# Performance work log

Measured on AMD Instinct MI355X. Metric: run time of the kernel, lower is better.

The kernel has to match this reference:

```python
import jax, jax.numpy as jnp
import numpy as np

# dims
B, H, W = 2, 128, 256
MD = 34            # model_dim (last 2 channels = sin/cos lat)
LD = MD - 2        # learnable_dim = 32
NH, HD = 4, 8      # n_heads, head_dim
SH = 64            # shared_hidden (DISCO out channels)
K = 25             # number of DISCO basis functions (5x5 kernel_shape)
P = 7              # local stencil width (lat x lon support of geodesic basis)
R = P // 2
FF1, FF2 = 512, 256


def setup_inputs() -> dict:
    key = jax.random.key(0)
    ks = jax.random.split(key, 16)
    x = jax.random.normal(ks[0], (B, H, W, MD), dtype=jnp.float32)
    # latitude-dependent sparse geodesic basis values over a 7x7 stencil
    psi_val = jax.random.uniform(ks[1], (K, H, P * P), dtype=jnp.float32) * 0.1
    disco_w = jax.random.normal(ks[2], (SH, K), dtype=jnp.float32) * 0.1
    disco_b = jax.random.normal(ks[3], (SH,), dtype=jnp.float32) * 0.01
    # per-head MLP: shared_hidden -> 32 -> 1
    hw1 = jax.random.normal(ks[4], (NH, SH, 32), dtype=jnp.float32) * (1.0 / np.sqrt(SH))
    hb1 = jax.random.normal(ks[5], (NH, 32), dtype=jnp.float32) * 0.01
    hw2 = jax.random.normal(ks[6], (NH, 32, 1), dtype=jnp.float32) * (1.0 / np.sqrt(32))
    hb2 = jax.random.normal(ks[7], (NH, 1), dtype=jnp.float32) * 0.01
    # FFN: model_dim -> 512 -> 256 -> learnable_dim
    fw1 = jax.random.normal(ks[8], (MD, FF1), dtype=jnp.float32) * (1.0 / np.sqrt(MD))
    fw1 = fw1.at[-2:, :].set(0.0)  # matches ffn[0].weight[:, -2:] = 0 init
    fb1 = jax.random.normal(ks[9], (FF1,), dtype=jnp.float32) * 0.01
    fw2 = jax.random.normal(ks[10], (FF1, FF2), dtype=jnp.float32) * (1.0 / np.sqrt(FF1))
    fb2 = jax.random.normal(ks[11], (FF2,), dtype=jnp.float32) * 0.01
    fw3 = jax.random.normal(ks[12], (FF2, LD), dtype=jnp.float32) * (1.0 / np.sqrt(FF2))
    fb3 = jax.random.normal(ks[13], (LD,), dtype=jnp.float32) * 0.01
    return {"x": x, "psi_val": psi_val, "disco_w": disco_w, "disco_b": disco_b,
            "hw1": hw1, "hb1": hb1, "hw2": hw2, "hb2": hb2,
            "fw1": fw1, "fb1": fb1, "fw2": fw2, "fb2": fb2, "fw3": fw3, "fb3": fb3}


def _gelu(t):
    return jax.nn.gelu(t, approximate=False)  # torch nn.GELU default (erf)


def _disco_s2(xn, psi_val, disco_w, disco_b):
    """DISCO sparse-basis conv on single-channel maps.
    xn: (N, H, W). Basis values vary with output latitude, longitude is
    translation-invariant; support is a lat-clamped / lon-wrapped 7x7 stencil.
    Returns (N, SH, H, W)."""
    xp = jnp.pad(xn, ((0, 0), (R, R), (0, 0)), mode="edge")  # clamp at poles
    shifts = []
    for dlat in range(P):
        row = xp[:, dlat:dlat + H, :]
        for dlon in range(-R, R + 1):
            shifts.append(jnp.roll(row, -dlon, axis=2))  # wrap in longitude
    xs = jnp.stack(shifts, axis=1)  # (N, P*P, H, W)
    basis = jnp.einsum("khp,nphw->nkhw", psi_val, xs)       # basis aggregation
    return jnp.einsum("fk,nkhw->nfhw", disco_w, basis) + disco_b[None, :, None, None]


def reference(x, psi_val, disco_w, disco_b, hw1, hb1, hw2, hb2,
              fw1, fb1, fw2, fb2, fw3, fb3):
    x_learn = x[..., :LD]
    sin_cos = x[..., LD:]
    x_res = x_learn
    # (B,H,W,LD) -> (B*LD, H, W): each learnable channel is a 1-channel map
    xn = x_learn.transpose(0, 3, 1, 2).reshape(B * LD, H, W)
    d = _disco_s2(xn, psi_val, disco_w, disco_b)              # (B*LD, SH, H, W)
    d = d.reshape(B, LD, SH, H, W).transpose(0, 3, 4, 1, 2)    # (B,H,W,LD,SH)
    # per-head MLP over its head_dim slice (head index is outer in LD)
    d = d.reshape(B, H, W, NH, HD, SH)
    h = _gelu(jnp.einsum("bxynds,nso->bxyndo", d, hw1) + hb1[None, None, None, :, None, :])
    h = jnp.einsum("bxyndo,noe->bxynde", h, hw2) + hb2[None, None, None, :, None, :]
    x_learn = h[..., 0].reshape(B, H, W, LD)
    x_learn = x_learn + x_res                                  # use_residual
    x_full = jnp.concatenate([x_learn, sin_cos], axis=-1)
    x_res2 = x_learn
    t = _gelu(x_full @ fw1 + fb1)
    t = _gelu(t @ fw2 + fb2)
    t = t @ fw3 + fb3                                          # dropout p=0 -> id
    x_learn = t + x_res2
    return jnp.concatenate([x_learn, sin_cos], axis=-1)
```

## Files before the change

kernel.cpp:

```cpp
#include <hip/hip_runtime.h>
#include <math.h>


typedef __attribute__((ext_vector_type(8))) short bfrag;
typedef __attribute__((ext_vector_type(4))) float ffrag;
typedef __attribute__((ext_vector_type(4))) short short4v;

union bfi4 { int4 i; bfrag b; };

__device__ __forceinline__ float gelu_f(float v) {
  const float z = v * (2.3022077484f + 0.1029451564f * v * v);
  const float e = __builtin_amdgcn_exp2f(-z);
  return v * __builtin_amdgcn_rcpf(1.0f + e);
}

__device__ __forceinline__ short f2bf(float f) {
  union { float f; unsigned u; } v; v.f = f;
  unsigned r = (v.u + 0x7fffu + ((v.u >> 16) & 1u)) >> 16;
  return (short)r;
}

__device__ __forceinline__ short f2bf_fast(float f) {
  union { float f; unsigned u; } v; v.f = f;
  return (short)((v.u + 0x8000u) >> 16);
}

__device__ __forceinline__ float bf2f(short s) {
  union { float f; unsigned u; } v;
  v.u = ((unsigned)(unsigned short)s) << 16;
  return v.f;
}

__device__ __forceinline__ int pkbf(float a, float b) {
  union { float f; unsigned u; } va, vb; va.f = a; vb.f = b;
  return (int)__builtin_amdgcn_perm(vb.u + 0x8000u, va.u + 0x8000u, 0x07060302u);
}

__device__ __forceinline__ void st4bf(short* p, float4 v) {
  short4v s;
  s[0] = f2bf(v.x); s[1] = f2bf(v.y); s[2] = f2bf(v.z); s[3] = f2bf(v.w);
  *(short4v*)p = s;
}

__device__ __forceinline__ void tile_map(int& w0, int& b, int& h, int& lin) {
  lin  = blockIdx.x + (blockIdx.y << 3) + (blockIdx.z << 10);
  const int xcd  = lin & 7;
  const int slot = lin >> 3;
  w0 = (slot & 7) * 32;
  b  = (slot >> 3) & 1;
  h  = (xcd << 4) | (slot >> 4);
}

__global__ __launch_bounds__(256) void k01_prep(
    const float* __restrict__ psi, const float* __restrict__ dw,
    const float* __restrict__ db,
    const float* __restrict__ fw1, const float* __restrict__ fw2,
    const float* __restrict__ fw3, const float* __restrict__ hw1,
    const float* __restrict__ hb1,
    short* __restrict__ wcb, short* __restrict__ fw1s,
    short* __restrict__ fw2s, short* __restrict__ fw3s) {
  __shared__ __align__(16) char sm[24960];
  const int bid = blockIdx.x;
  const int tid = threadIdx.x;

  if (bid < 512) {
    float* tileL  = (float*)sm;
    float* hw1n   = (float*)(sm + 13312);
    short* tile2  = (short*)(sm + 21504);
    float* bias32 = (float*)(sm + 24832);
    const int h = bid >> 2;
    const int n = bid & 3;
    const int lane = tid & 63;
    const int w = __builtin_amdgcn_readfirstlane(tid >> 6);

    for (int e = tid; e < 512; e += 256)
      ((float4*)hw1n)[e] = ((const float4*)(hw1 + n * 2048))[e];

    float dwreg[25];
#pragma unroll
    for (int kk = 0; kk < 25; ++kk) dwreg[kk] = dw[lane * 25 + kk];
    const int p0 = w * 13;
    const int pend = (p0 + 13 < 49) ? (p0 + 13) : 49;
#pragma unroll 1
    for (int p = p0; p < pend; ++p) {
      float ae = 0.f, ao = 0.f;
#pragma unroll
      for (int kk = 0; kk < 24; kk += 2) {
        ae += dwreg[kk]     * psi[kk * 6272 + h * 49 + p];
        ao += dwreg[kk + 1] * psi[(kk + 1) * 6272 + h * 49 + p];
      }
      ae += dwreg[24] * psi[24 * 6272 + h * 49 + p];
      tileL[lane * 52 + p] = ae + ao;
    }
    __syncthreads();

    if (tid >= 224) {
      const int o = tid - 224;
      float acc = hb1[n * 32 + o];
#pragma unroll 4
      for (int s = 0; s < 64; ++s) acc += hw1n[s * 32 + o] * db[s];
      bias32[o] = acc;
    }

    const int o = tid & 31;
#pragma unroll 1
    for (int pp = tid >> 5; pp < 25; pp += 8) {
      const int p2 = pp * 2;
      float a0 = 0.f, a1 = 0.f, a2 = 0.f, a3 = 0.f;
#pragma unroll 4
      for (int f = 0; f < 64; f += 2) {
        const float wv0 = hw1n[f * 32 + o];
        const float wv1 = hw1n[(f + 1) * 32 + o];
        a0 += wv0 * tileL[f * 52 + p2];
        a1 += wv0 * tileL[f * 52 + p2 + 1];
        a2 += wv1 * tileL[(f + 1) * 52 + p2];
        a3 += wv1 * tileL[(f + 1) * 52 + p2 + 1];
      }
      tile2[o * 52 + p2] = f2bf(a0 + a2);
      if (p2 + 1 < 49) tile2[o * 52 + p2 + 1] = f2bf(a1 + a3);
    }
    __syncthreads();

    short* outp = wcb + h * 16384 + n * 4096;
    for (int idx = tid; idx < 4096; idx += 256) {
      const int jj = idx & 7, ln = (idx >> 3) & 63;
      const int nt = (idx >> 9) & 1, kt = (idx >> 10) & 1;
      const int par = idx >> 11;
      const int k = kt * 32 + ((ln >> 4) << 3) + jj;
      const int oo = nt * 16 + (ln & 15);
      const int r = k >> 3, dlt = k & 7;
      const int j = par ? (dlt - 1) : dlt;
      short v = 0;
      if (r < 7 && j >= 0 && j < 7) v = tile2[oo * 52 + r * 7 + j];
      if (k == 56) v = f2bf(bias32[oo]);
      outp[idx] = v;
    }
    return;
  }

  if (bid < 528) {
    short* S = (short*)sm;
    const int kt = bid - 512;
    const float* src = fw2 + kt * 8192;
    for (int q = tid; q < 2048; q += 256) {
      const int lin = q * 4;
      const int kk = lin >> 8, nn = lin & 255;
      st4bf(S + kk * 260 + nn, *(const float4*)(src + lin));
    }
    __syncthreads();
    short* dst = fw2s + kt * 8192;
    for (int q = tid; q < 8192; q += 256) {
      const int jj = q & 7, lane = (q >> 3) & 63, nt = q >> 9;
      const int kk = (lane >> 4) * 8 + jj, nn = nt * 16 + (lane & 15);
      dst[q] = S[kk * 260 + nn];
    }
    return;
  }

  if (bid < 530) {
    const int X = bid - 528;
    short* S = (short*)sm;
    for (int q = tid; q < 2048; q += 256) {
      const int lin = q * 4;
      const int kk = lin >> 8, nn = lin & 255;
      st4bf(S + kk * 260 + nn, *(const float4*)(fw1 + kk * 512 + X * 256 + nn));
    }
    __syncthreads();
    for (int q = tid; q < 8192; q += 256) {
      const int jj = q & 7, lane = (q >> 3) & 63, ntl = q >> 9;
      const int kk = (lane >> 4) * 8 + jj, nn = ntl * 16 + (lane & 15);
      fw1s[X * 8192 + q] = S[kk * 260 + nn];
    }
    return;
  }

  {
    short* S = (short*)sm;
    for (int q = tid; q < 2048; q += 256) {
      const int lin = q * 4;
      const int kk = lin >> 5, nn = lin & 31;
      st4bf(S + kk * 36 + nn, *(const float4*)(fw3 + lin));
    }
    __syncthreads();
    for (int q = tid; q < 8192; q += 256) {
      const int jj = q & 7, lane = (q >> 3) & 63;
      const int nt = (q >> 9) & 1, kt = q >> 10;
      const int kk = kt * 32 + (lane >> 4) * 8 + jj, nn = nt * 16 + (lane & 15);
      fw3s[q] = S[kk * 36 + nn];
    }
  }
}

__global__ __launch_bounds__(256, 8) void k23_fused(
    const float* __restrict__ x,    const short* __restrict__ wcb,
    const float* __restrict__ hw2,  const float* __restrict__ hb2,
    const short* __restrict__ fw1s, const short* __restrict__ fw2s,
    const short* __restrict__ fw3s,
    const float* __restrict__ fb1,  const float* __restrict__ fb2,
    const float* __restrict__ fb3,  float* __restrict__ outb) {
  __shared__ __align__(16) char smem[20384];
  short* sX = (short*)smem;
  short* sM = (short*)(smem + 18080);

  const int tid = threadIdx.x;
  int w0, b, h, lin;
  tile_map(w0, b, h, lin);

  const int lane = tid & 63, lm = lane & 15, lq = lane >> 4;
  const int n = tid >> 6;
  const int idx16 = (lane ^ 16) << 2;
  const int idx32 = (lane ^ 32) << 2;
  const unsigned injm = (lq == 3) ? 0xFFFFu : 0u;

  const float hb2n = hb2[n];

  {
    int4* p = (int4*)smem;
    int4 z; z.x = z.y = z.z = z.w = 0;
    for (int e = tid; e < 20384 / 16; e += 256) p[e] = z;
  }
  __syncthreads();

#pragma unroll 1
  for (int r = 0; r < 7; ++r) {
    int hr = h - 3 + r; hr = hr < 0 ? 0 : (hr > 127 ? 127 : hr);
    const int slot = (r < 4) ? (2 * r) : (2 * r - 7);
    const float* __restrict__ xrow = x + (size_t)((b * 128 + hr) * 256) * 34;
    short* __restrict__ sxr = sX + slot * 40;
    for (int e = tid; e < 39 * 16; e += 256) {
      const int c2 = e & 15;
      const int wp = e >> 4;
      const int wr = (w0 - 3 + wp) & 255;
      const float2 v = *(const float2*)&xrow[wr * 34 + c2 * 2];
      short* dp = sxr + (c2 * 2) * 280 + wp;
      dp[0]   = f2bf_fast(v.x);
      dp[280] = f2bf_fast(v.y);
    }
  }
  __syncthreads();

  const int* tpB = (const int*)sX;

  const float4 w0v = *(const float4*)(hw2 + n * 32 + lq * 4);
  const float4 w1v = *(const float4*)(hw2 + n * 32 + 16 + lq * 4);

#pragma unroll 1
  for (int par = 0; par < 2; ++par) {
    bfrag cw[2][2];
#pragma unroll
    for (int kt = 0; kt < 2; ++kt)
#pragma unroll
      for (int nt = 0; nt < 2; ++nt)
        cw[kt][nt] = *(const bfrag*)(wcb + h * 16384 + n * 4096 +
                         ((par * 2 + kt) * 2 + nt) * 512 + lane * 8);

#pragma unroll 1
    for (int i = 0; i < 8; ++i) {
      const int c = n * 8 + i;

      const int base0 = c * 140 + lq * 40 + lm;
      bfi4 u0, u1;
      u0.i.x = tpB[base0];      u0.i.y = tpB[base0 + 1];
      u0.i.z = tpB[base0 + 2];  u0.i.w = tpB[base0 + 3];
      u1.i.x = tpB[base0 + 20]; u1.i.y = tpB[base0 + 21];
      u1.i.z = tpB[base0 + 22]; u1.i.w = tpB[base0 + 23];
      u1.i.x = (int)(((unsigned)u1.i.x & ~injm) | (0x3F80u & injm));

      ffrag h0 = {0.f, 0.f, 0.f, 0.f}, h1 = {0.f, 0.f, 0.f, 0.f};
      h0 = __builtin_amdgcn_mfma_f32_16x16x32_bf16(cw[0][0], u0.b, h0, 0, 0, 0);
      h0 = __builtin_amdgcn_mfma_f32_16x16x32_bf16(cw[1][0], u1.b, h0, 0, 0, 0);
      h1 = __builtin_amdgcn_mfma_f32_16x16x32_bf16(cw[0][1], u0.b, h1, 0, 0, 0);
      h1 = __builtin_amdgcn_mfma_f32_16x16x32_bf16(cw[1][1], u1.b, h1, 0, 0, 0);

      float s0 = gelu_f(h0[0]) * w0v.x;
      s0 += gelu_f(h0[1]) * w0v.y;
      s0 += gelu_f(h0[2]) * w0v.z;
      s0 += gelu_f(h0[3]) * w0v.w;
      float s1 = gelu_f(h1[0]) * w1v.x;
      s1 += gelu_f(h1[1]) * w1v.y;
      s1 += gelu_f(h1[2]) * w1v.z;
      s1 += gelu_f(h1[3]) * w1v.w;
      union { float f; int i; } sv, t1, t2;
      sv.f = s0 + s1;
      t1.i = __builtin_amdgcn_ds_bpermute(idx16, sv.i);
      sv.f += t1.f;
      t2.i = __builtin_amdgcn_ds_bpermute(idx32, sv.i);
      const float tot = sv.f + t2.f;

      const int p = 2 * lm + par;
      const float res = bf2f(sX[c * 280 + 243 + p]);
      if (lq == 0) sM[p * 36 + c] = f2bf_fast(tot + hb2n + res);
    }
  }
  __syncthreads();

  short* sT1h = (short*)smem;
  short* sT2  = (short*)smem;
  float* sO   = (float*)smem;
  const int wave = n;
  const int koff = lq * 8;
  const int mt3 = wave & 1;
  const int nt3 = wave >> 1;
  const int col3 = nt3 * 16 + lm;
  const int pixg = (b * 128 + h) * 256 + w0;
  const int n0 = wave * 4;

  ffrag acc[2][4];
#pragma unroll
  for (int mt = 0; mt < 2; ++mt)
#pragma unroll
    for (int ni = 0; ni < 4; ++ni) acc[mt][ni] = ffrag{0.f, 0.f, 0.f, 0.f};
  const short* w2base = fw2s + n0 * 512 + lane * 8;

#pragma unroll 1
  for (int H = 0; H < 2; ++H) {
#pragma unroll
    for (int ni = 0; ni < 4; ++ni) {
      const bfrag b1f = *(const bfrag*)(fw1s +
                          (H * 16 + wave * 4 + ni) * 512 + lane * 8);
      const int ntl = wave * 4 + ni;
      const float4 fb1v = *(const float4*)(fb1 + H * 256 + ntl * 16 + lq * 4);
#pragma unroll
      for (int mt = 0; mt < 2; ++mt) {
        const bfrag aFm = *(const bfrag*)(sM + (mt * 16 + lm) * 36 + koff);
        ffrag cc = {0.f, 0.f, 0.f, 0.f};
        cc = __builtin_amdgcn_mfma_f32_16x16x32_bf16(b1f, aFm, cc, 0, 0, 0);
        int2 wv;
        wv.x = pkbf(gelu_f(cc[0] + fb1v.x), gelu_f(cc[1] + fb1v.y));
        wv.y = pkbf(gelu_f(cc[2] + fb1v.z), gelu_f(cc[3] + fb1v.w));
        *(int2*)(sT1h + (mt * 16 + lm) * 264 + ntl * 16 + lq * 4) = wv;
      }
    }
    __syncthreads();

#pragma unroll 1
    for (int kt = 0; kt < 8; ++kt) {
      const bfrag a0 = *(const bfrag*)(sT1h + lm * 264 + kt * 32 + koff);
      const bfrag a1 = *(const bfrag*)(sT1h + (16 + lm) * 264 + kt * 32 + koff);
#pragma unroll
      for (int np = 0; np < 2; ++np) {
        const bfrag bv0 = *(const bfrag*)(w2base + (H * 8 + kt) * 8192 + (2 * np) * 512);
        const bfrag bv1 = *(const bfrag*)(w2base + (H * 8 + kt) * 8192 + (2 * np + 1) * 512);
        acc[0][2 * np]     = __builtin_amdgcn_mfma_f32_16x16x32_bf16(bv0, a0, acc[0][2 * np], 0, 0, 0);
        acc[1][2 * np]     = __builtin_amdgcn_mfma_f32_16x16x32_bf16(bv0, a1, acc[1][2 * np], 0, 0, 0);
        acc[0][2 * np + 1] = __builtin_amdgcn_mfma_f32_16x16x32_bf16(bv1, a0, acc[0][2 * np + 1], 0, 0, 0);
        acc[1][2 * np + 1] = __builtin_amdgcn_mfma_f32_16x16x32_bf16(bv1, a1, acc[1][2 * np + 1], 0, 0, 0);
      }
    }
    __syncthreads();
  }

#pragma unroll
  for (int mt = 0; mt < 2; ++mt)
#pragma unroll
    for (int ni = 0; ni < 4; ++ni) {
      const float4 fb2v = *(const float4*)(fb2 + (n0 + ni) * 16 + lq * 4);
      int2 wv;
      wv.x = pkbf(gelu_f(acc[mt][ni][0] + fb2v.x), gelu_f(acc[mt][ni][1] + fb2v.y));
      wv.y = pkbf(gelu_f(acc[mt][ni][2] + fb2v.z), gelu_f(acc[mt][ni][3] + fb2v.w));
      *(int2*)(sT2 + (mt * 16 + lm) * 264 + (n0 + ni) * 16 + lq * 4) = wv;
    }
  __syncthreads();

  ffrag c3 = {0.f, 0.f, 0.f, 0.f};
  const short* sA3 = sT2 + (mt3 * 16 + lm) * 264 + koff;
#pragma unroll
  for (int kt = 0; kt < 8; ++kt) {
    const bfrag a = *(const bfrag*)(sA3 + kt * 32);
    const bfrag bw = *(const bfrag*)(fw3s + nt3 * 512 + kt * 1024 + lane * 8);
    c3 = __builtin_amdgcn_mfma_f32_16x16x32_bf16(a, bw, c3, 0, 0, 0);
  }
  __syncthreads();
  {
    const float bias = fb3[col3];
#pragma unroll
    for (int r = 0; r < 4; ++r) {
      const int row = mt3 * 16 + lq * 4 + r;
      const float res = bf2f(sM[row * 36 + col3]);
      sO[row * 34 + col3] = c3[r] + bias + res;
    }
  }
  if (tid < 32) {
    const float2 scv =
        *(const float2*)&x[(size_t)(((b * 128 + h) * 256 + w0 + tid)) * 34 + 32];
    sO[tid * 34 + 32] = scv.x;
    sO[tid * 34 + 33] = scv.y;
  }
  __syncthreads();
  {
    const float4* sp = (const float4*)sO;
    float4* dp = (float4*)(outb + (size_t)pixg * 34);
    for (int e = tid; e < 272; e += 256) dp[e] = sp[e];
  }
}

extern "C" void kernel_launch(void* const* d_in, const int* in_sizes, int n_in,
                              void* d_out, int out_size, void* d_ws, size_t ws_size,
                              hipStream_t stream) {
  const float* x   = (const float*)d_in[0];
  const float* psi = (const float*)d_in[1];
  const float* dw  = (const float*)d_in[2];
  const float* db  = (const float*)d_in[3];
  const float* hw1 = (const float*)d_in[4];
  const float* hb1 = (const float*)d_in[5];
  const float* hw2 = (const float*)d_in[6];
  const float* hb2 = (const float*)d_in[7];
  const float* fw1 = (const float*)d_in[8];
  const float* fb1 = (const float*)d_in[9];
  const float* fw2 = (const float*)d_in[10];
  const float* fb2 = (const float*)d_in[11];
  const float* fw3 = (const float*)d_in[12];
  const float* fb3 = (const float*)d_in[13];
  float* outb = (float*)d_out;

  short* wcb  = (short*)d_ws;
  short* fw1s = wcb + 2097152;
  short* fw2s = fw1s + 16384;
  short* fw3s = fw2s + 131072;

  hipLaunchKernelGGL(k01_prep, dim3(531), dim3(256), 0, stream,
                     psi, dw, db, fw1, fw2, fw3, hw1, hb1,
                     wcb, fw1s, fw2s, fw3s);
  hipLaunchKernelGGL(k23_fused, dim3(8, 128, 2), dim3(256), 0, stream,
                     x, wcb, hw2, hb2,
                     fw1s, fw2s, fw3s, fb1, fb2, fb3, outb);
}
```

Before: 163.8 us.

## Split prep weight-combine blocks by output half, stage psi in LDS, trim zero-fill

The prep kernel now launches twice as many combine blocks, each handling 16 of the 32 head-MLP outputs, so more CUs share the per-latitude basis/weight folding. Psi values are staged once into shared memory instead of being re-read from global memory by every wave, and hw1 is stored with a padded stride to avoid bank conflicts. The fused kernel no longer zero-fills its whole shared buffer with a barrier; it zeroes only a small tail region. The risk is that some region the kernel relied on being zero is no longer cleared. It also duplicates the basis combine work across the two halves.

```diff
diff --git a/kernel.cpp b/kernel.cpp
--- a/kernel.cpp
+++ b/kernel.cpp
@@ -59,26 +59,36 @@
     const float* __restrict__ hb1,
     short* __restrict__ wcb, short* __restrict__ fw1s,
     short* __restrict__ fw2s, short* __restrict__ fw3s) {
-  __shared__ __align__(16) char sm[24960];
+  __shared__ __align__(16) char sm[24832];
   const int bid = blockIdx.x;
   const int tid = threadIdx.x;
 
-  if (bid < 512) {
-    float* tileL  = (float*)sm;
-    float* hw1n   = (float*)(sm + 13312);
-    short* tile2  = (short*)(sm + 21504);
-    float* bias32 = (float*)(sm + 24832);
-    const int h = bid >> 2;
-    const int n = bid & 3;
+  if (bid < 1024) {
+    float* psL    = (float*)sm;
+    float* tileL  = (float*)(sm + 5200);
+    float* hw1h   = (float*)(sm + 18512);
+    short* tile2  = (short*)(sm + 22864);
+    float* bias16 = (float*)(sm + 24528);
+    const int h = bid >> 3;
+    const int n = (bid >> 1) & 3;
+    const int G = bid & 1;
     const int lane = tid & 63;
     const int w = __builtin_amdgcn_readfirstlane(tid >> 6);
 
-    for (int e = tid; e < 512; e += 256)
-      ((float4*)hw1n)[e] = ((const float4*)(hw1 + n * 2048))[e];
+    for (int e = tid; e < 1600; e += 256) {
+      const int kk = e >> 6, p = e & 63;
+      if (p < 49) psL[kk * 52 + p] = psi[kk * 6272 + h * 49 + p];
+    }
+    for (int e = tid; e < 1024; e += 256) {
+      const int f = e >> 4, o = e & 15;
+      hw1h[f * 17 + o] = hw1[n * 2048 + f * 32 + G * 16 + o];
+    }
 
     float dwreg[25];
 #pragma unroll
     for (int kk = 0; kk < 25; ++kk) dwreg[kk] = dw[lane * 25 + kk];
+    __syncthreads();
+
     const int p0 = w * 13;
     const int pend = (p0 + 13 < 49) ? (p0 + 13) : 49;
 #pragma unroll 1
@@ -86,31 +96,31 @@
       float ae = 0.f, ao = 0.f;
 #pragma unroll
       for (int kk = 0; kk < 24; kk += 2) {
-        ae += dwreg[kk]     * psi[kk * 6272 + h * 49 + p];
-        ao += dwreg[kk + 1] * psi[(kk + 1) * 6272 + h * 49 + p];
+        ae += dwreg[kk]     * psL[kk * 52 + p];
+        ao += dwreg[kk + 1] * psL[(kk + 1) * 52 + p];
       }
-      ae += dwreg[24] * psi[24 * 6272 + h * 49 + p];
+      ae += dwreg[24] * psL[24 * 52 + p];
       tileL[lane * 52 + p] = ae + ao;
     }
     __syncthreads();
 
-    if (tid >= 224) {
-      const int o = tid - 224;
-      float acc = hb1[n * 32 + o];
+    if (tid >= 240) {
+      const int o = tid - 240;
+      float acc = hb1[n * 32 + G * 16 + o];
 #pragma unroll 4
-      for (int s = 0; s < 64; ++s) acc += hw1n[s * 32 + o] * db[s];
-      bias32[o] = acc;
-    }
-
-    const int o = tid & 31;
-#pragma unroll 1
-    for (int pp = tid >> 5; pp < 25; pp += 8) {
+      for (int s = 0; s < 64; ++s) acc += hw1h[s * 17 + o] * db[s];
+      bias16[o] = acc;
+    }
+
+    const int o = tid & 15;
+#pragma unroll 1
+    for (int pp = tid >> 4; pp < 25; pp += 16) {
       const int p2 = pp * 2;
       float a0 = 0.f, a1 = 0.f, a2 = 0.f, a3 = 0.f;
 #pragma unroll 4
       for (int f = 0; f < 64; f += 2) {
-        const float wv0 = hw1n[f * 32 + o];
-        const float wv1 = hw1n[(f + 1) * 32 + o];
+        const float wv0 = hw1h[f * 17 + o];
+        const float wv1 = hw1h[(f + 1) * 17 + o];
         a0 += wv0 * tileL[f * 52 + p2];
         a1 += wv0 * tileL[f * 52 + p2 + 1];
         a2 += wv1 * tileL[(f + 1) * 52 + p2];
@@ -122,25 +132,26 @@
     __syncthreads();
 
     short* outp = wcb + h * 16384 + n * 4096;
-    for (int idx = tid; idx < 4096; idx += 256) {
-      const int jj = idx & 7, ln = (idx >> 3) & 63;
-      const int nt = (idx >> 9) & 1, kt = (idx >> 10) & 1;
-      const int par = idx >> 11;
+    for (int q = tid; q < 2048; q += 256) {
+      const int sub = q & 511;
+      const int pk = q >> 9;
+      const int par = pk >> 1, kt = pk & 1;
+      const int jj = sub & 7, ln = (sub >> 3) & 63;
       const int k = kt * 32 + ((ln >> 4) << 3) + jj;
-      const int oo = nt * 16 + (ln & 15);
+      const int ol = ln & 15;
       const int r = k >> 3, dlt = k & 7;
       const int j = par ? (dlt - 1) : dlt;
       short v = 0;
-      if (r < 7 && j >= 0 && j < 7) v = tile2[oo * 52 + r * 7 + j];
-      if (k == 56) v = f2bf(bias32[oo]);
-      outp[idx] = v;
+      if (r < 7 && j >= 0 && j < 7) v = tile2[ol * 52 + r * 7 + j];
+      if (k == 56) v = f2bf(bias16[ol]);
+      outp[par * 2048 + kt * 1024 + G * 512 + sub] = v;
     }
     return;
   }
 
-  if (bid < 528) {
+  if (bid < 1040) {
     short* S = (short*)sm;
-    const int kt = bid - 512;
+    const int kt = bid - 1024;
     const float* src = fw2 + kt * 8192;
     for (int q = tid; q < 2048; q += 256) {
       const int lin = q * 4;
@@ -157,8 +168,8 @@
     return;
   }
 
-  if (bid < 530) {
-    const int X = bid - 528;
+  if (bid < 1042) {
+    const int X = bid - 1040;
     short* S = (short*)sm;
     for (int q = tid; q < 2048; q += 256) {
       const int lin = q * 4;
@@ -214,12 +225,10 @@
 
   const float hb2n = hb2[n];
 
-  {
-    int4* p = (int4*)smem;
+  if (tid < 10) {
     int4 z; z.x = z.y = z.z = z.w = 0;
-    for (int e = tid; e < 20384 / 16; e += 256) p[e] = z;
-  }
-  __syncthreads();
+    ((int4*)(smem + 17920))[tid] = z;
+  }
 
 #pragma unroll 1
   for (int r = 0; r < 7; ++r) {
@@ -418,7 +427,7 @@
   short* fw2s = fw1s + 16384;
   short* fw3s = fw2s + 131072;
 
-  hipLaunchKernelGGL(k01_prep, dim3(531), dim3(256), 0, stream,
+  hipLaunchKernelGGL(k01_prep, dim3(1043), dim3(256), 0, stream,
                      psi, dw, db, fw1, fw2, fw3, hw1, hb1,
                      wcb, fw1s, fw2s, fw3s);
   hipLaunchKernelGGL(k23_fused, dim3(8, 128, 2), dim3(256), 0, stream,
```

After: 164.0 us (median of 2 runs). About the same (+0.1%).
